# Optimization experiments

Hardware: AMD Instinct MI355X
Metric: run time of the kernel (lower is better)

The kernel has to match this reference:

```python
import jax, jax.numpy as jnp
import numpy as np

LMAX_IN = 3
LMAX_OUT = 3
C = 64          # num_channel
H = 64          # num_channel_hidden
N_NODES = 2048
N_EDGES = 8192

# All coupled (l1, l2, l3) paths with |l1-l2| <= l3 <= min(l1+l2, lmax_out)
COMBS = [(l1, l2, l3)
         for l1 in range(LMAX_IN + 1)
         for l2 in range(LMAX_OUT + 1)
         for l3 in range(abs(l1 - l2), min(l1 + l2, LMAX_OUT) + 1)]
COUNTS = {l3: sum(1 for c in COMBS if c[2] == l3) for l3 in range(LMAX_OUT + 1)}

# Fixed coupling (Clebsch-Gordan-like) tensors for each path, shape (2l1+1, 2l2+1, 2l3+1).
# Deterministic constants (not trained / not differentiated), standing in for the
# e3nn CG coefficients used by InterEinsumTC.
_rng = np.random.RandomState(1234)
CG = [jnp.asarray((_rng.randn(2 * l1 + 1, 2 * l2 + 1, 2 * l3 + 1) * 0.2).astype(np.float32))
      for (l1, l2, l3) in COMBS]


def setup_inputs() -> dict:
    key = jax.random.key(0)
    ks = jax.random.split(key, 16)
    inp = {}
    for l in range(LMAX_OUT + 1):
        inp[f"x{l}"] = jax.random.normal(ks[l], (N_NODES, C, 2 * l + 1), dtype=jnp.float32)
        inp[f"y{l}"] = jax.random.normal(ks[4 + l], (N_EDGES, 2 * l + 1), dtype=jnp.float32)
        fan_in = C * COUNTS[l]
        inp[f"w_lin{l}"] = jax.random.normal(ks[8 + l], (fan_in, H), dtype=jnp.float32) / np.float32(np.sqrt(fan_in))
    inp["ws"] = jax.random.normal(ks[12], (N_EDGES, C * len(COMBS)), dtype=jnp.float32)
    inp["edge_index"] = jax.random.randint(ks[13], (2, N_EDGES), 0, N_NODES, dtype=jnp.int32)
    return inp


def _forward(x0, x1, x2, x3, y0, y1, y2, y3, ws, w_lin0, w_lin1, w_lin2, w_lin3, edge_index):
    xs = (x0, x1, x2, x3)
    ys = (y0, y1, y2, y3)
    wl = (w_lin0, w_lin1, w_lin2, w_lin3)
    src, dst = edge_index[0], edge_index[1]
    # per-edge gather of node features for every input degree
    xg = [x[src] for x in xs]                      # [E, C, 2l1+1]
    buf = {l3: [] for l3 in range(LMAX_OUT + 1)}
    for i, (l1, l2, l3) in enumerate(COMBS):
        # tensor-product contraction: [E, C, 2l3+1]
        out = jnp.einsum('lmn,ecl,em->ecn', CG[i], xg[l1], ys[l2])
        w = ws[:, i * C:(i + 1) * C][:, :, None]   # [E, C, 1] per-path per-channel weight
        buf[l3].append(w * out)
    res = []
    for l3 in range(LMAX_OUT + 1):
        m_ji = jnp.concatenate(buf[l3], axis=1)    # [E, C*count_l3, 2l3+1]
        m_i = jax.ops.segment_sum(m_ji, dst, num_segments=N_NODES)  # scatter-sum -> [N, C*count, 2l3+1]
        res.append(jnp.einsum('ncm,ch->nhm', m_i, wl[l3]))          # per-l3 linear -> [N, H, 2l3+1]
    return tuple(res)


def reference(x0, x1, x2, x3, y0, y1, y2, y3, ws, w_lin0, w_lin1, w_lin2, w_lin3, edge_index):
    return _forward(x0, x1, x2, x3, y0, y1, y2, y3, ws,
                    w_lin0, w_lin1, w_lin2, w_lin3, edge_index)
```

## Files before the change

kernel.cpp:

```cpp
#include <hip/hip_runtime.h>
#include <hip/hip_bf16.h>
#include <cmath>
#include <cstdint>

#define NNODES 2048
#define NEDGES 8192
#define NCH 64
#define NHID 64
#define NPATH 34
#define NTASK (NPATH * NCH)
#define CGTOT 3436
#define MROW 9984
#define TTOT2 888
#define EBLK 8

#define MI_BYTES ((size_t)NNODES * MROW * 2)
#define XT_BYTES ((size_t)NNODES * 16 * NCH * 2)
#define OFF_OFF  (MI_BYTES)
#define CUR_OFF  (OFF_OFF + 2052 * 4)
#define PACK_OFF (CUR_OFF + 2048 * 4)
#define ORD_OFF  (PACK_OFF + 8192 * 4)
#define XT_OFF   (ORD_OFF + 2048 * 4)
#define CGP_OFF  (XT_OFF + XT_BYTES)
#define CGP_FLOATS (TTOT2 * 9)

typedef __attribute__((ext_vector_type(8))) short short8;
typedef __attribute__((ext_vector_type(4))) float floatx4;

struct PathTables {
  int l1[NPATH], l2[NPATH], l3[NPATH];
  int cg_off[NPATH], t_off2[NPATH], rank[NPATH];
  int gpaths[2][20], gnp[2], gbase[2], glen[2];
  int cg_total, ttot2, npaths;
};

constexpr PathTables make_tables() {
  PathTables tb{};
  int np = 0;
  for (int a = 0; a < 4; ++a)
    for (int b = 0; b < 4; ++b) {
      int lo = a > b ? a - b : b - a;
      int hi = a + b < 3 ? a + b : 3;
      for (int c = lo; c <= hi; ++c) { tb.l1[np] = a; tb.l2[np] = b; tb.l3[np] = c; ++np; }
    }
  int cg = 0;
  int cnt[4] = {0, 0, 0, 0};
  for (int i = 0; i < np; ++i) {
    tb.cg_off[i] = cg; tb.rank[i] = cnt[tb.l3[i]]++;
    cg += (2 * tb.l1[i] + 1) * (2 * tb.l2[i] + 1) * (2 * tb.l3[i] + 1);
  }
  int tt2 = 0;
  for (int g = 0; g < 2; ++g) {
    tb.gbase[g] = tt2;
    for (int i = 0; i < np; ++i) {
      int gi = (tb.l3[i] == 0 || tb.l3[i] == 3) ? 0 : 1;
      if (gi != g) continue;
      tb.gpaths[g][tb.gnp[g]++] = i;
      tb.t_off2[i] = tt2;
      int d1 = 2 * tb.l1[i] + 1, d3 = 2 * tb.l3[i] + 1;
      tt2 += ((d1 * d3 + 7) / 8) * 8;
    }
    tb.glen[g] = tt2 - tb.gbase[g];
  }
  tb.cg_total = cg; tb.ttot2 = tt2; tb.npaths = np;
  return tb;
}

constexpr PathTables H_TB = make_tables();
static_assert(H_TB.npaths == NPATH, "npaths");
static_assert(H_TB.cg_total == CGTOT, "cgtot");
static_assert(H_TB.ttot2 == TTOT2, "ttot2");
static_assert(H_TB.gnp[0] == 14 && H_TB.gnp[1] == 20, "gnp");
static_assert(H_TB.gbase[1] == 432 && H_TB.glen[1] == 456, "gsplit");

__constant__ PathTables d_tb = make_tables();

namespace {
struct MT19937 {
  uint32_t mt[624]; int mti; bool has_g; double gval;
  void seed(uint32_t s) {
    for (int i = 0; i < 624; ++i) { mt[i] = s; s = 1812433253u * (s ^ (s >> 30)) + (uint32_t)i + 1u; }
    mti = 624; has_g = false; gval = 0.0;
  }
  uint32_t next() {
    if (mti >= 624) {
      for (int i = 0; i < 624; ++i) {
        uint32_t y = (mt[i] & 0x80000000u) | (mt[(i + 1) % 624] & 0x7fffffffu);
        mt[i] = mt[(i + 397) % 624] ^ (y >> 1) ^ ((y & 1u) ? 0x9908b0dfu : 0u);
      }
      mti = 0;
    }
    uint32_t y = mt[mti++];
    y ^= y >> 11; y ^= (y << 7) & 0x9d2c5680u; y ^= (y << 15) & 0xefc60000u; y ^= y >> 18;
    return y;
  }
  double rdbl() {
    uint32_t a = next() >> 5, b = next() >> 6;
    return ((double)a * 67108864.0 + (double)b) / 9007199254740992.0;
  }
  double gauss() {
    if (has_g) { has_g = false; return gval; }
    double x1, x2, r2;
    do {
      x1 = 2.0 * rdbl() - 1.0;
      x2 = 2.0 * rdbl() - 1.0;
      r2 = x1 * x1 + x2 * x2;
    } while (r2 >= 1.0 || r2 == 0.0);
    double f = std::sqrt(-2.0 * std::log(r2) / r2);
    gval = f * x1; has_g = true;
    return f * x2;
  }
};

float host_pack[CGP_FLOATS];
float* g_cg_dev = nullptr;
bool g_cg_ok = false;

struct CGInit {
  CGInit() {
    static float cg[CGTOT];
    MT19937 g; g.seed(1234u);
    int idx = 0;
    for (int i = 0; i < NPATH; ++i) {
      int d1 = 2 * H_TB.l1[i] + 1, d2 = 2 * H_TB.l2[i] + 1, d3 = 2 * H_TB.l3[i] + 1;
      int sz = d1 * d2 * d3;
      for (int k = 0; k < sz; ++k) cg[idx++] = (float)(g.gauss() * 0.2);
    }
    const int ybase[4] = {0, 1, 4, 9};
    for (int k = 0; k < CGP_FLOATS; ++k) host_pack[k] = 0.f;
    for (int i = 0; i < NPATH; ++i) {
      int d1 = 2 * H_TB.l1[i] + 1, d2 = 2 * H_TB.l2[i] + 1, d3 = 2 * H_TB.l3[i] + 1;
      for (int l = 0; l < d1; ++l)
        for (int n3 = 0; n3 < d3; ++n3) {
          int tt2 = H_TB.t_off2[i] + l * d3 + n3;
          for (int m = 0; m < d2; ++m)
            host_pack[tt2 * 8 + m] = cg[H_TB.cg_off[i] + l * d2 * d3 + m * d3 + n3];
          host_pack[TTOT2 * 8 + tt2] = (float)ybase[H_TB.l2[i]];
        }
    }
    (void)hipHostRegister(host_pack, sizeof(host_pack), hipHostRegisterDefault);
    void* p = nullptr;
    if (hipMalloc(&p, sizeof(host_pack)) == hipSuccess && p) {
      if (hipMemcpy(p, host_pack, sizeof(host_pack), hipMemcpyHostToDevice) == hipSuccess) {
        float back = -1.f;
        if (hipMemcpy(&back, (float*)p + (CGP_FLOATS - 1), sizeof(float),
                      hipMemcpyDeviceToHost) == hipSuccess && back == host_pack[CGP_FLOATS - 1]) {
          g_cg_dev = (float*)p;
          g_cg_ok = true;
        }
      }
    }
  }
} cg_init_instance;
}

__device__ __forceinline__ float bf2f(unsigned short u) {
  union { unsigned int i; float f; } v; v.i = ((unsigned int)u) << 16; return v.f;
}
__device__ __forceinline__ unsigned short f2bf(float f) {
  __hip_bfloat16 h = __float2bfloat16(f);
  union { __hip_bfloat16 h; unsigned short u; } v; v.h = h; return v.u;
}

__global__ __launch_bounds__(1024) void scan_kernel(
    const int* __restrict__ edge_index, int* __restrict__ off, int* __restrict__ cursor,
    int* __restrict__ order)
{
  __shared__ int ldeg[NNODES];
  __shared__ int csum[1024];
  __shared__ int hist[64];
  const int t = threadIdx.x;
  for (int i = t; i < NNODES; i += 1024) ldeg[i] = 0;
  __syncthreads();
  const int* __restrict__ dsts = edge_index + NEDGES;
  for (int e = t; e < NEDGES; e += 1024) atomicAdd(&ldeg[dsts[e]], 1);
  __syncthreads();
  const int l0 = ldeg[2 * t], l1 = ldeg[2 * t + 1];
  const int s = l0 + l1;
  csum[t] = s;
  __syncthreads();
  for (int o = 1; o < 1024; o <<= 1) {
    int v = (t >= o) ? csum[t - o] : 0;
    __syncthreads();
    csum[t] += v;
    __syncthreads();
  }
  int run = csum[t] - s;
  off[2 * t] = run; cursor[2 * t] = run;
  off[2 * t + 1] = run + l0; cursor[2 * t + 1] = run + l0;
  if (t == 0) off[NNODES] = NEDGES;
  if (t < 64) hist[t] = 0;
  __syncthreads();
  for (int i = t; i < NNODES; i += 1024) {
    int d = ldeg[i]; d = d > 63 ? 63 : d;
    atomicAdd(&hist[63 - d], 1);
  }
  __syncthreads();
  if (t == 0) { int r2 = 0; for (int b = 0; b < 64; ++b) { int c = hist[b]; hist[b] = r2; r2 += c; } }
  __syncthreads();
  for (int i = t; i < NNODES; i += 1024) {
    int d = ldeg[i]; d = d > 63 ? 63 : d;
    int pos = atomicAdd(&hist[63 - d], 1);
    order[pos] = i;
  }
}

__global__ __launch_bounds__(256) void fill_xt_kernel(
    const int* __restrict__ edge_index, int* __restrict__ cursor, int* __restrict__ pack,
    const float* __restrict__ x0, const float* __restrict__ x1,
    const float* __restrict__ x2, const float* __restrict__ x3,
    __hip_bfloat16* __restrict__ xT)
{
  const int b = blockIdx.x;
  const int t = threadIdx.x;
  if (b < 32) {
    const int e = b * 256 + t;
    const int d = edge_index[NEDGES + e];
    const int s = edge_index[e];
    const int pos = atomicAdd(&cursor[d], 1);
    pack[pos] = e | (s << 13);
  } else {
    const int n = b - 32;
    for (int idx = t; idx < 1024; idx += 256) {
      const int j = idx >> 6, c = idx & 63;
      const float* src; int d1, m;
      if (j < 1)      { src = x0; d1 = 1; m = j; }
      else if (j < 4) { src = x1; d1 = 3; m = j - 1; }
      else if (j < 9) { src = x2; d1 = 5; m = j - 4; }
      else            { src = x3; d1 = 7; m = j - 9; }
      const float v = src[((size_t)n * NCH + c) * d1 + m];
      xT[((size_t)n * 16 + j) * NCH + c] = __float2bfloat16(v);
    }
  }
}

template <int D1, int D3>
__device__ __forceinline__ void tp_task_run(
    int wcol, int toff_l, int rank, int nb, const int* __restrict__ epk,
    const float (*Ts)[456], const float* __restrict__ ws,
    const unsigned short* __restrict__ xT,
    int n, bool first, __hip_bfloat16* __restrict__ m_out)
{
  constexpr int Kc = (D3 == 1) ? 256 : (D3 == 3) ? 576 : (D3 == 5) ? 704 : 640;
  constexpr int Rc = (D3 == 1) ? 0 : (D3 == 3) ? 256 : (D3 == 5) ? 1984 : 5504;
  constexpr int JB = (D1 == 1) ? 0 : (D1 == 3) ? 1 : (D1 == 5) ? 4 : 9;
  const int c = wcol & 63;

  float wv_[EBLK];
#pragma unroll
  for (int ei = 0; ei < EBLK; ++ei)
    wv_[ei] = (ei < nb) ? ws[(size_t)(epk[ei] & 8191) * NTASK + wcol] : 0.f;

  float acc[D3];
#pragma unroll
  for (int m = 0; m < D3; ++m) acc[m] = 0.f;

  for (int ei = 0; ei < nb; ++ei) {
    const int s = epk[ei] >> 13;
    const unsigned short* __restrict__ xr = xT + ((size_t)s * 16 + JB) * NCH + c;
    const float* __restrict__ Tp = &Ts[ei][toff_l];
    float u[D3];
#pragma unroll
    for (int m = 0; m < D3; ++m) u[m] = 0.f;
#pragma unroll
    for (int l = 0; l < D1; ++l) {
      const float xv = bf2f(xr[l * NCH]);
#pragma unroll
      for (int m = 0; m < D3; ++m) u[m] += xv * Tp[l * D3 + m];
    }
#pragma unroll
    for (int m = 0; m < D3; ++m) acc[m] += wv_[ei] * u[m];
  }

  __hip_bfloat16* mo = m_out + (size_t)n * MROW + Rc + rank * NCH + c;
  if (first) {
#pragma unroll
    for (int m = 0; m < D3; ++m) mo[m * Kc] = __float2bfloat16(acc[m]);
  } else {
#pragma unroll
    for (int m = 0; m < D3; ++m)
      mo[m * Kc] = __float2bfloat16(__bfloat162float(mo[m * Kc]) + acc[m]);
  }
}

__global__ __launch_bounds__(256) void tp_node_kernel(
    const float* __restrict__ y0, const float* __restrict__ y1,
    const float* __restrict__ y2, const float* __restrict__ y3,
    const float* __restrict__ ws, const unsigned short* __restrict__ xT,
    const float* __restrict__ cg_pack,
    const int* __restrict__ off, const int* __restrict__ pack,
    const int* __restrict__ order,
    __hip_bfloat16* __restrict__ m_out)
{
  __shared__ float Ts[EBLK][456];
  __shared__ float y_s[EBLK][18];
  __shared__ int epk[EBLK];

  const int bid = blockIdx.x;
  const int n = order[bid >> 1];
  const int g = bid & 1;
  const int t = threadIdx.x;
  const int beg = off[n];
  const int cnt = off[n + 1] - beg;
  const int gbase = d_tb.gbase[g];
  const int glen  = d_tb.glen[g];
  const int ntask = d_tb.gnp[g] << 6;
  const float* __restrict__ metaf = cg_pack + TTOT2 * 8;

  for (int base = 0; base == 0 || base < cnt; base += EBLK) {
    int nb = cnt - base;
    nb = nb < 0 ? 0 : (nb > EBLK ? EBLK : nb);
    if (t < nb) epk[t] = pack[beg + base + t];
    if (t >= 64 && t < 64 + 2 * EBLK) y_s[(t - 64) >> 1][16 + (t & 1)] = 0.f;
    __syncthreads();
    if (t < nb * 16) {
      const int ei = t >> 4, j = t & 15;
      const int e = epk[ei] & 8191;
      float v;
      if (j < 1)      v = y0[e];
      else if (j < 4) v = y1[e * 3 + (j - 1)];
      else if (j < 9) v = y2[e * 5 + (j - 4)];
      else            v = y3[e * 7 + (j - 9)];
      y_s[ei][j] = v;
    }
    __syncthreads();
    for (int ei = 0; ei < nb; ++ei) {
      for (int j = t; j < glen; j += 256) {
        const int tt2 = gbase + j;
        const float4 a = *(const float4*)(cg_pack + tt2 * 8);
        const float4 c4 = *(const float4*)(cg_pack + tt2 * 8 + 4);
        const int yb = (int)metaf[tt2];
        const float* yy = &y_s[ei][yb];
        Ts[ei][j] = a.x * yy[0] + a.y * yy[1] + a.z * yy[2] + a.w * yy[3]
                  + c4.x * yy[4] + c4.y * yy[5] + c4.z * yy[6] + c4.w * yy[7];
      }
    }
    __syncthreads();

    const bool first = (base == 0);
    for (int k = 0; k * 256 + t < ntask; ++k) {
      const int tl = k * 256 + t;
      const int i = d_tb.gpaths[g][tl >> 6];
      const int wcol = (i << 6) | (tl & 63);
      const int toff_l = d_tb.t_off2[i] - gbase;
      const int rk = d_tb.rank[i];
      const int code = d_tb.l1[i] * 4 + d_tb.l3[i];
      switch (code) {
        case  0: tp_task_run<1,1>(wcol, toff_l, rk, nb, epk, Ts, ws, xT, n, first, m_out); break;
        case  1: tp_task_run<1,3>(wcol, toff_l, rk, nb, epk, Ts, ws, xT, n, first, m_out); break;
        case  2: tp_task_run<1,5>(wcol, toff_l, rk, nb, epk, Ts, ws, xT, n, first, m_out); break;
        case  3: tp_task_run<1,7>(wcol, toff_l, rk, nb, epk, Ts, ws, xT, n, first, m_out); break;
        case  4: tp_task_run<3,1>(wcol, toff_l, rk, nb, epk, Ts, ws, xT, n, first, m_out); break;
        case  5: tp_task_run<3,3>(wcol, toff_l, rk, nb, epk, Ts, ws, xT, n, first, m_out); break;
        case  6: tp_task_run<3,5>(wcol, toff_l, rk, nb, epk, Ts, ws, xT, n, first, m_out); break;
        case  7: tp_task_run<3,7>(wcol, toff_l, rk, nb, epk, Ts, ws, xT, n, first, m_out); break;
        case  8: tp_task_run<5,1>(wcol, toff_l, rk, nb, epk, Ts, ws, xT, n, first, m_out); break;
        case  9: tp_task_run<5,3>(wcol, toff_l, rk, nb, epk, Ts, ws, xT, n, first, m_out); break;
        case 10: tp_task_run<5,5>(wcol, toff_l, rk, nb, epk, Ts, ws, xT, n, first, m_out); break;
        case 11: tp_task_run<5,7>(wcol, toff_l, rk, nb, epk, Ts, ws, xT, n, first, m_out); break;
        case 12: tp_task_run<7,1>(wcol, toff_l, rk, nb, epk, Ts, ws, xT, n, first, m_out); break;
        case 13: tp_task_run<7,3>(wcol, toff_l, rk, nb, epk, Ts, ws, xT, n, first, m_out); break;
        case 14: tp_task_run<7,5>(wcol, toff_l, rk, nb, epk, Ts, ws, xT, n, first, m_out); break;
        default: tp_task_run<7,7>(wcol, toff_l, rk, nb, epk, Ts, ws, xT, n, first, m_out); break;
      }
    }
    __syncthreads();
  }
}

template <int D3, int K, int ROFF>
__device__ __forceinline__ void lin_mfma_body(
    int blk, const unsigned short* __restrict__ mu, const float* __restrict__ wl,
    float* __restrict__ out, unsigned short (*A_s)[72], unsigned short (*W_s)[72])
{
  const int t = threadIdx.x;
  const int wv = t >> 6;
  const int lane = t & 63;
  const int idx16 = lane & 15;
  const int quad = lane >> 4;
  const int r0 = blk * 64;

  floatx4 acc[4] = {{0.f,0.f,0.f,0.f},{0.f,0.f,0.f,0.f},{0.f,0.f,0.f,0.f},{0.f,0.f,0.f,0.f}};

  for (int k0 = 0; k0 < K; k0 += 64) {
    for (int idx = t; idx < 512; idx += 256) {
      const int rr = idx >> 3, ck = (idx & 7) * 8;
      const int r = r0 + rr;
      const int nn = r / D3, mm = r - nn * D3;
      const uint4 v = *(const uint4*)(mu + (size_t)nn * MROW + ROFF + mm * K + k0 + ck);
      *(uint4*)&A_s[rr][ck] = v;
    }
    {
      const int h = t & 63, kg = t >> 6;
      unsigned short tmp[16];
#pragma unroll
      for (int j = 0; j < 16; ++j)
        tmp[j] = f2bf(wl[(size_t)(k0 + kg * 16 + j) * 64 + h]);
      *(uint4*)&W_s[h][kg * 16]     = *(const uint4*)&tmp[0];
      *(uint4*)&W_s[h][kg * 16 + 8] = *(const uint4*)&tmp[8];
    }
    __syncthreads();
#pragma unroll
    for (int ks = 0; ks < 2; ++ks) {
      const int kb = ks * 32 + quad * 8;
      const short8 af = *(const short8*)&A_s[wv * 16 + idx16][kb];
#pragma unroll
      for (int nt = 0; nt < 4; ++nt) {
        const short8 bf = *(const short8*)&W_s[nt * 16 + idx16][kb];
        acc[nt] = __builtin_amdgcn_mfma_f32_16x16x32_bf16(af, bf, acc[nt], 0, 0, 0);
      }
    }
    __syncthreads();
  }

#pragma unroll
  for (int nt = 0; nt < 4; ++nt) {
    const int h = nt * 16 + idx16;
#pragma unroll
    for (int r = 0; r < 4; ++r) {
      const int row = r0 + wv * 16 + quad * 4 + r;
      const int nn = row / D3, mm = row - nn * D3;
      out[((size_t)nn * NHID + h) * D3 + mm] = acc[nt][r];
    }
  }
}

__global__ __launch_bounds__(256) void lin_fused_kernel(
    const unsigned short* __restrict__ mu,
    const float* __restrict__ wl0, const float* __restrict__ wl1,
    const float* __restrict__ wl2, const float* __restrict__ wl3,
    float* __restrict__ out)
{
  __shared__ unsigned short A_s[64][72];
  __shared__ unsigned short W_s[64][72];
  const int b = blockIdx.x;
  if (b < 32)       lin_mfma_body<1, 256, 0>   (b,       mu, wl0, out,           A_s, W_s);
  else if (b < 128) lin_mfma_body<3, 576, 256> (b - 32,  mu, wl1, out + 131072,  A_s, W_s);
  else if (b < 288) lin_mfma_body<5, 704, 1984>(b - 128, mu, wl2, out + 524288,  A_s, W_s);
  else              lin_mfma_body<7, 640, 5504>(b - 288, mu, wl3, out + 1179648, A_s, W_s);
}

extern "C" void kernel_launch(void* const* d_in, const int* in_sizes, int n_in,
                              void* d_out, int out_size, void* d_ws, size_t ws_size,
                              hipStream_t stream) {
  const float* x0  = (const float*)d_in[0];
  const float* y0  = (const float*)d_in[1];
  const float* wl0 = (const float*)d_in[2];
  const float* x1  = (const float*)d_in[3];
  const float* y1  = (const float*)d_in[4];
  const float* wl1 = (const float*)d_in[5];
  const float* x2  = (const float*)d_in[6];
  const float* y2  = (const float*)d_in[7];
  const float* wl2 = (const float*)d_in[8];
  const float* x3  = (const float*)d_in[9];
  const float* y3  = (const float*)d_in[10];
  const float* wl3 = (const float*)d_in[11];
  const float* ws  = (const float*)d_in[12];
  const int* edge_index = (const int*)d_in[13];
  float* out = (float*)d_out;

  __hip_bfloat16* m_i = (__hip_bfloat16*)d_ws;
  int* csr_off = (int*)((char*)d_ws + OFF_OFF);
  int* cursor  = (int*)((char*)d_ws + CUR_OFF);
  int* pack    = (int*)((char*)d_ws + PACK_OFF);
  int* order   = (int*)((char*)d_ws + ORD_OFF);
  __hip_bfloat16* xT = (__hip_bfloat16*)((char*)d_ws + XT_OFF);

  const float* cg_pack;
  if (g_cg_ok) {
    cg_pack = g_cg_dev;
  } else {
    float* cg_ws = (float*)((char*)d_ws + CGP_OFF);
    hipMemcpyAsync(cg_ws, host_pack, sizeof(host_pack), hipMemcpyHostToDevice, stream);
    cg_pack = cg_ws;
  }

  scan_kernel<<<1, 1024, 0, stream>>>(edge_index, csr_off, cursor, order);
  fill_xt_kernel<<<32 + NNODES, 256, 0, stream>>>(edge_index, cursor, pack,
                                                  x0, x1, x2, x3, xT);
  tp_node_kernel<<<2 * NNODES, 256, 0, stream>>>(y0, y1, y2, y3, ws,
                                                 (const unsigned short*)xT, cg_pack,
                                                 csr_off, pack, order, m_i);
  lin_fused_kernel<<<512, 256, 0, stream>>>((const unsigned short*)m_i,
                                            wl0, wl1, wl2, wl3, out);
}
```

Before: 233.5 us.

## Pad CG tables for vector LDS reads and pretranspose linear weights to bf16

```diff
diff --git a/kernel.cpp b/kernel.cpp
--- a/kernel.cpp
+++ b/kernel.cpp
@@ -11,27 +11,30 @@
 #define NTASK (NPATH * NCH)
 #define CGTOT 3436
 #define MROW 9984
-#define TTOT2 888
+#define TT3 1028
 #define EBLK 8
+#define GLEN_MAX 564
 
 #define MI_BYTES ((size_t)NNODES * MROW * 2)
 #define XT_BYTES ((size_t)NNODES * 16 * NCH * 2)
+#define WT_BYTES ((size_t)64 * NTASK * 2)
 #define OFF_OFF  (MI_BYTES)
 #define CUR_OFF  (OFF_OFF + 2052 * 4)
 #define PACK_OFF (CUR_OFF + 2048 * 4)
 #define ORD_OFF  (PACK_OFF + 8192 * 4)
 #define XT_OFF   (ORD_OFF + 2048 * 4)
-#define CGP_OFF  (XT_OFF + XT_BYTES)
-#define CGP_FLOATS (TTOT2 * 9)
+#define WT_OFF   (XT_OFF + XT_BYTES)
+#define CGP_OFF  (WT_OFF + WT_BYTES)
+#define CGP_FLOATS (TT3 * 9)
 
 typedef __attribute__((ext_vector_type(8))) short short8;
 typedef __attribute__((ext_vector_type(4))) float floatx4;
 
 struct PathTables {
   int l1[NPATH], l2[NPATH], l3[NPATH];
-  int cg_off[NPATH], t_off2[NPATH], rank[NPATH];
-  int gpaths[2][20], gnp[2], gbase[2], glen[2];
-  int cg_total, ttot2, npaths;
+  int cg_off[NPATH], t_off3[NPATH], rank[NPATH];
+  int gpaths[2][20], gnp[2], gbase3[2], glen3[2];
+  int cg_total, tt3, npaths;
 };
 
 constexpr PathTables make_tables() {
@@ -49,29 +52,30 @@
     tb.cg_off[i] = cg; tb.rank[i] = cnt[tb.l3[i]]++;
     cg += (2 * tb.l1[i] + 1) * (2 * tb.l2[i] + 1) * (2 * tb.l3[i] + 1);
   }
-  int tt2 = 0;
+  int tt = 0;
   for (int g = 0; g < 2; ++g) {
-    tb.gbase[g] = tt2;
+    tb.gbase3[g] = tt;
     for (int i = 0; i < np; ++i) {
       int gi = (tb.l3[i] == 0 || tb.l3[i] == 3) ? 0 : 1;
       if (gi != g) continue;
       tb.gpaths[g][tb.gnp[g]++] = i;
-      tb.t_off2[i] = tt2;
+      tb.t_off3[i] = tt;
       int d1 = 2 * tb.l1[i] + 1, d3 = 2 * tb.l3[i] + 1;
-      tt2 += ((d1 * d3 + 7) / 8) * 8;
-    }
-    tb.glen[g] = tt2 - tb.gbase[g];
-  }
-  tb.cg_total = cg; tb.ttot2 = tt2; tb.npaths = np;
+      int st = (d3 <= 4) ? 4 : 8;
+      tt += d1 * st;
+    }
+    tb.glen3[g] = tt - tb.gbase3[g];
+  }
+  tb.cg_total = cg; tb.tt3 = tt; tb.npaths = np;
   return tb;
 }
 
 constexpr PathTables H_TB = make_tables();
 static_assert(H_TB.npaths == NPATH, "npaths");
 static_assert(H_TB.cg_total == CGTOT, "cgtot");
-static_assert(H_TB.ttot2 == TTOT2, "ttot2");
+static_assert(H_TB.tt3 == TT3, "tt3");
 static_assert(H_TB.gnp[0] == 14 && H_TB.gnp[1] == 20, "gnp");
-static_assert(H_TB.gbase[1] == 432 && H_TB.glen[1] == 456, "gsplit");
+static_assert(H_TB.gbase3[1] == 464 && H_TB.glen3[0] == 464 && H_TB.glen3[1] == 564, "gsplit");
 
 __constant__ PathTables d_tb = make_tables();
 
@@ -130,12 +134,13 @@
     for (int k = 0; k < CGP_FLOATS; ++k) host_pack[k] = 0.f;
     for (int i = 0; i < NPATH; ++i) {
       int d1 = 2 * H_TB.l1[i] + 1, d2 = 2 * H_TB.l2[i] + 1, d3 = 2 * H_TB.l3[i] + 1;
+      int st = (d3 <= 4) ? 4 : 8;
       for (int l = 0; l < d1; ++l)
         for (int n3 = 0; n3 < d3; ++n3) {
-          int tt2 = H_TB.t_off2[i] + l * d3 + n3;
+          int slot = H_TB.t_off3[i] + l * st + n3;
           for (int m = 0; m < d2; ++m)
-            host_pack[tt2 * 8 + m] = cg[H_TB.cg_off[i] + l * d2 * d3 + m * d3 + n3];
-          host_pack[TTOT2 * 8 + tt2] = (float)ybase[H_TB.l2[i]];
+            host_pack[slot * 8 + m] = cg[H_TB.cg_off[i] + l * d2 * d3 + m * d3 + n3];
+          host_pack[TT3 * 8 + slot] = (float)ybase[H_TB.l2[i]];
         }
     }
     (void)hipHostRegister(host_pack, sizeof(host_pack), hipHostRegisterDefault);
@@ -209,7 +214,9 @@
     const int* __restrict__ edge_index, int* __restrict__ cursor, int* __restrict__ pack,
     const float* __restrict__ x0, const float* __restrict__ x1,
     const float* __restrict__ x2, const float* __restrict__ x3,
-    __hip_bfloat16* __restrict__ xT)
+    const float* __restrict__ wl0, const float* __restrict__ wl1,
+    const float* __restrict__ wl2, const float* __restrict__ wl3,
+    __hip_bfloat16* __restrict__ xT, unsigned short* __restrict__ wt_all)
 {
   const int b = blockIdx.x;
   const int t = threadIdx.x;
@@ -219,7 +226,7 @@
     const int s = edge_index[e];
     const int pos = atomicAdd(&cursor[d], 1);
     pack[pos] = e | (s << 13);
-  } else {
+  } else if (b < 32 + NNODES) {
     const int n = b - 32;
     for (int idx = t; idx < 1024; idx += 256) {
       const int j = idx >> 6, c = idx & 63;
@@ -231,19 +238,30 @@
       const float v = src[((size_t)n * NCH + c) * d1 + m];
       xT[((size_t)n * 16 + j) * NCH + c] = __float2bfloat16(v);
     }
+  } else {
+    const int b3 = b - (32 + NNODES);
+    const int k = b3 * 4 + (t >> 6);
+    const int h = t & 63;
+    const float* src; int K, base, kl;
+    if (k < 256)       { src = wl0; K = 256; base = 0;     kl = k; }
+    else if (k < 832)  { src = wl1; K = 576; base = 16384; kl = k - 256; }
+    else if (k < 1536) { src = wl2; K = 704; base = 53248; kl = k - 832; }
+    else               { src = wl3; K = 640; base = 98304; kl = k - 1536; }
+    wt_all[base + h * K + kl] = f2bf(src[(size_t)kl * 64 + h]);
   }
 }
 
 template <int D1, int D3>
 __device__ __forceinline__ void tp_task_run(
     int wcol, int toff_l, int rank, int nb, const int* __restrict__ epk,
-    const float (*Ts)[456], const float* __restrict__ ws,
+    const float (*Ts)[GLEN_MAX], const float* __restrict__ ws,
     const unsigned short* __restrict__ xT,
     int n, bool first, __hip_bfloat16* __restrict__ m_out)
 {
   constexpr int Kc = (D3 == 1) ? 256 : (D3 == 3) ? 576 : (D3 == 5) ? 704 : 640;
   constexpr int Rc = (D3 == 1) ? 0 : (D3 == 3) ? 256 : (D3 == 5) ? 1984 : 5504;
   constexpr int JB = (D1 == 1) ? 0 : (D1 == 3) ? 1 : (D1 == 5) ? 4 : 9;
+  constexpr int ST = (D3 <= 4) ? 4 : 8;
   const int c = wcol & 63;
 
   float wv_[EBLK];
@@ -265,8 +283,12 @@
 #pragma unroll
     for (int l = 0; l < D1; ++l) {
       const float xv = bf2f(xr[l * NCH]);
-#pragma unroll
-      for (int m = 0; m < D3; ++m) u[m] += xv * Tp[l * D3 + m];
+      const floatx4 r0 = *(const floatx4*)(Tp + l * ST);
+      floatx4 r1;
+      if (D3 > 4) r1 = *(const floatx4*)(Tp + l * ST + 4);
+#pragma unroll
+      for (int m = 0; m < D3; ++m)
+        u[m] += xv * ((m < 4) ? r0[m] : r1[m - 4]);
     }
 #pragma unroll
     for (int m = 0; m < D3; ++m) acc[m] += wv_[ei] * u[m];
@@ -292,7 +314,7 @@
     const int* __restrict__ order,
     __hip_bfloat16* __restrict__ m_out)
 {
-  __shared__ float Ts[EBLK][456];
+  __shared__ float Ts[EBLK][GLEN_MAX];
   __shared__ float y_s[EBLK][18];
   __shared__ int epk[EBLK];
 
@@ -302,10 +324,10 @@
   const int t = threadIdx.x;
   const int beg = off[n];
   const int cnt = off[n + 1] - beg;
-  const int gbase = d_tb.gbase[g];
-  const int glen  = d_tb.glen[g];
+  const int gbase = d_tb.gbase3[g];
+  const int glen  = d_tb.glen3[g];
   const int ntask = d_tb.gnp[g] << 6;
-  const float* __restrict__ metaf = cg_pack + TTOT2 * 8;
+  const float* __restrict__ metaf = cg_pack + TT3 * 8;
 
   for (int base = 0; base == 0 || base < cnt; base += EBLK) {
     int nb = cnt - base;
@@ -326,10 +348,10 @@
     __syncthreads();
     for (int ei = 0; ei < nb; ++ei) {
       for (int j = t; j < glen; j += 256) {
-        const int tt2 = gbase + j;
-        const float4 a = *(const float4*)(cg_pack + tt2 * 8);
-        const float4 c4 = *(const float4*)(cg_pack + tt2 * 8 + 4);
-        const int yb = (int)metaf[tt2];
+        const int slot = gbase + j;
+        const float4 a = *(const float4*)(cg_pack + slot * 8);
+        const float4 c4 = *(const float4*)(cg_pack + slot * 8 + 4);
+        const int yb = (int)metaf[slot];
         const float* yy = &y_s[ei][yb];
         Ts[ei][j] = a.x * yy[0] + a.y * yy[1] + a.z * yy[2] + a.w * yy[3]
                   + c4.x * yy[4] + c4.y * yy[5] + c4.z * yy[6] + c4.w * yy[7];
@@ -342,7 +364,7 @@
       const int tl = k * 256 + t;
       const int i = d_tb.gpaths[g][tl >> 6];
       const int wcol = (i << 6) | (tl & 63);
-      const int toff_l = d_tb.t_off2[i] - gbase;
+      const int toff_l = d_tb.t_off3[i] - gbase;
       const int rk = d_tb.rank[i];
       const int code = d_tb.l1[i] * 4 + d_tb.l3[i];
       switch (code) {
@@ -370,47 +392,29 @@
 
 template <int D3, int K, int ROFF>
 __device__ __forceinline__ void lin_mfma_body(
-    int blk, const unsigned short* __restrict__ mu, const float* __restrict__ wl,
-    float* __restrict__ out, unsigned short (*A_s)[72], unsigned short (*W_s)[72])
+    int blk, const unsigned short* __restrict__ mu, const unsigned short* __restrict__ wt,
+    float* __restrict__ out)
 {
   const int t = threadIdx.x;
   const int wv = t >> 6;
   const int lane = t & 63;
   const int idx16 = lane & 15;
   const int quad = lane >> 4;
-  const int r0 = blk * 64;
+
+  const int arow = blk * 64 + wv * 16 + idx16;
+  const int ann = arow / D3, amm = arow - ann * D3;
+  const unsigned short* __restrict__ ap = mu + (size_t)ann * MROW + ROFF + amm * K + quad * 8;
+  const unsigned short* __restrict__ bp = wt + idx16 * K + quad * 8;
 
   floatx4 acc[4] = {{0.f,0.f,0.f,0.f},{0.f,0.f,0.f,0.f},{0.f,0.f,0.f,0.f},{0.f,0.f,0.f,0.f}};
 
-  for (int k0 = 0; k0 < K; k0 += 64) {
-    for (int idx = t; idx < 512; idx += 256) {
-      const int rr = idx >> 3, ck = (idx & 7) * 8;
-      const int r = r0 + rr;
-      const int nn = r / D3, mm = r - nn * D3;
-      const uint4 v = *(const uint4*)(mu + (size_t)nn * MROW + ROFF + mm * K + k0 + ck);
-      *(uint4*)&A_s[rr][ck] = v;
-    }
-    {
-      const int h = t & 63, kg = t >> 6;
-      unsigned short tmp[16];
-#pragma unroll
-      for (int j = 0; j < 16; ++j)
-        tmp[j] = f2bf(wl[(size_t)(k0 + kg * 16 + j) * 64 + h]);
-      *(uint4*)&W_s[h][kg * 16]     = *(const uint4*)&tmp[0];
-      *(uint4*)&W_s[h][kg * 16 + 8] = *(const uint4*)&tmp[8];
-    }
-    __syncthreads();
-#pragma unroll
-    for (int ks = 0; ks < 2; ++ks) {
-      const int kb = ks * 32 + quad * 8;
-      const short8 af = *(const short8*)&A_s[wv * 16 + idx16][kb];
-#pragma unroll
-      for (int nt = 0; nt < 4; ++nt) {
-        const short8 bf = *(const short8*)&W_s[nt * 16 + idx16][kb];
-        acc[nt] = __builtin_amdgcn_mfma_f32_16x16x32_bf16(af, bf, acc[nt], 0, 0, 0);
-      }
-    }
-    __syncthreads();
+  for (int k0 = 0; k0 < K; k0 += 32) {
+    const short8 af = *(const short8*)(ap + k0);
+#pragma unroll
+    for (int nt = 0; nt < 4; ++nt) {
+      const short8 bf = *(const short8*)(bp + nt * 16 * K + k0);
+      acc[nt] = __builtin_amdgcn_mfma_f32_16x16x32_bf16(af, bf, acc[nt], 0, 0, 0);
+    }
   }
 
 #pragma unroll
@@ -418,7 +422,7 @@
     const int h = nt * 16 + idx16;
 #pragma unroll
     for (int r = 0; r < 4; ++r) {
-      const int row = r0 + wv * 16 + quad * 4 + r;
+      const int row = blk * 64 + wv * 16 + quad * 4 + r;
       const int nn = row / D3, mm = row - nn * D3;
       out[((size_t)nn * NHID + h) * D3 + mm] = acc[nt][r];
     }
@@ -426,18 +430,14 @@
 }
 
 __global__ __launch_bounds__(256) void lin_fused_kernel(
-    const unsigned short* __restrict__ mu,
-    const float* __restrict__ wl0, const float* __restrict__ wl1,
-    const float* __restrict__ wl2, const float* __restrict__ wl3,
+    const unsigned short* __restrict__ mu, const unsigned short* __restrict__ wt_all,
     float* __restrict__ out)
 {
-  __shared__ unsigned short A_s[64][72];
-  __shared__ unsigned short W_s[64][72];
   const int b = blockIdx.x;
-  if (b < 32)       lin_mfma_body<1, 256, 0>   (b,       mu, wl0, out,           A_s, W_s);
-  else if (b < 128) lin_mfma_body<3, 576, 256> (b - 32,  mu, wl1, out + 131072,  A_s, W_s);
-  else if (b < 288) lin_mfma_body<5, 704, 1984>(b - 128, mu, wl2, out + 524288,  A_s, W_s);
-  else              lin_mfma_body<7, 640, 5504>(b - 288, mu, wl3, out + 1179648, A_s, W_s);
+  if (b < 32)       lin_mfma_body<1, 256, 0>   (b,       mu, wt_all,         out);
+  else if (b < 128) lin_mfma_body<3, 576, 256> (b - 32,  mu, wt_all + 16384, out + 131072);
+  else if (b < 288) lin_mfma_body<5, 704, 1984>(b - 128, mu, wt_all + 53248, out + 524288);
+  else              lin_mfma_body<7, 640, 5504>(b - 288, mu, wt_all + 98304, out + 1179648);
 }
 
 extern "C" void kernel_launch(void* const* d_in, const int* in_sizes, int n_in,
@@ -465,6 +465,7 @@
   int* pack    = (int*)((char*)d_ws + PACK_OFF);
   int* order   = (int*)((char*)d_ws + ORD_OFF);
   __hip_bfloat16* xT = (__hip_bfloat16*)((char*)d_ws + XT_OFF);
+  unsigned short* wt_all = (unsigned short*)((char*)d_ws + WT_OFF);
 
   const float* cg_pack;
   if (g_cg_ok) {
@@ -476,11 +477,12 @@
   }
 
   scan_kernel<<<1, 1024, 0, stream>>>(edge_index, csr_off, cursor, order);
-  fill_xt_kernel<<<32 + NNODES, 256, 0, stream>>>(edge_index, cursor, pack,
-                                                  x0, x1, x2, x3, xT);
+  fill_xt_kernel<<<32 + NNODES + 544, 256, 0, stream>>>(edge_index, cursor, pack,
+                                                        x0, x1, x2, x3,
+                                                        wl0, wl1, wl2, wl3,
+                                                        xT, wt_all);
   tp_node_kernel<<<2 * NNODES, 256, 0, stream>>>(y0, y1, y2, y3, ws,
                                                  (const unsigned short*)xT, cg_pack,
                                                  csr_off, pack, order, m_i);
-  lin_fused_kernel<<<512, 256, 0, stream>>>((const unsigned short*)m_i,
-                                            wl0, wl1, wl2, wl3, out);
-}
+  lin_fused_kernel<<<512, 256, 0, stream>>>((const unsigned short*)m_i, wt_all, out);
+}
```

After: 244.0 us. 1.05x slower.
